# Kernel tuning notes

Hardware: AMD Instinct MI355X
Metric: run time of the kernel (lower is better)

The kernel has to match this reference:

```python
import jax, jax.numpy as jnp
import numpy as np

N = 50000      # nodes
E = 800000     # edges
F_IN = 128     # num_node_features
H = 128        # hidden_size
P = 128        # projection_dim
G = 512        # num graphs in batch


def setup_inputs() -> dict:
    key = jax.random.key(0)
    ks = jax.random.split(key, 16)
    def w(k, shape, fan_in):
        return (jax.random.normal(k, shape, jnp.float32) / np.float32(np.sqrt(fan_in)))
    inp = {
        "x": jax.random.normal(ks[0], (N, F_IN), jnp.float32),
        "edge_index": jax.random.randint(ks[1], (2, E), 0, N, dtype=jnp.int32),
        "batch": jnp.sort(jax.random.randint(ks[2], (N,), 0, G, dtype=jnp.int32)),
        "W_in": w(ks[3], (F_IN, H), F_IN), "b_in": jnp.zeros((H,), jnp.float32),
        "W1": w(ks[4], (H, H), H), "b1": jnp.zeros((H,), jnp.float32),
        "W2": w(ks[5], (H, H), H), "b2": jnp.zeros((H,), jnp.float32),
        "W3": w(ks[6], (H, H), H), "b3": jnp.zeros((H,), jnp.float32),
        "Wp1": w(ks[7], (3 * H, H), 3 * H), "bp1": jnp.zeros((H,), jnp.float32),
        "Wp2": w(ks[8], (H, P), H), "bp2": jnp.zeros((P,), jnp.float32),
    }
    return inp


def _gcn_conv(h_in, W, b, src, dst, dis):
    # GCNConv: D^-1/2 (A+I) D^-1/2 (X W) + b, edge weights = 1
    h = h_in @ W                                        # [N,H]
    norm = (dis[src] * dis[dst])[:, None]               # [E,1]
    msg = h[src] * norm                                 # gather + scale
    agg = jax.ops.segment_sum(msg, dst, num_segments=N)  # scatter-add
    agg = agg + h * (dis * dis)[:, None]                 # self-loop term
    return agg + b


def reference(x, edge_index, batch, W_in, b_in, W1, b1, W2, b2, W3, b3, Wp1, bp1, Wp2, bp2):
    src, dst = edge_index[0], edge_index[1]
    # degree with self-loops (target-side, symmetric norm)
    deg = jax.ops.segment_sum(jnp.ones((E,), jnp.float32), dst, num_segments=N) + 1.0
    dis = jax.lax.rsqrt(deg)                             # deg^-1/2, deg >= 1

    h = x @ W_in + b_in                                  # input projection
    r1 = jax.nn.relu(h + _gcn_conv(h, W1, b1, src, dst, dis))   # dropout = id (eval)
    r2 = jax.nn.relu(r1 + _gcn_conv(r1, W2, b2, src, dst, dis))
    r3 = jax.nn.relu(r2 + _gcn_conv(r2, W3, b3, src, dst, dis))

    jk = jnp.concatenate([r1, r2, r3], axis=1)           # JumpingKnowledge 'cat' -> [N,3H]
    sums = jax.ops.segment_sum(jk, batch, num_segments=G)
    cnts = jax.ops.segment_sum(jnp.ones((N,), jnp.float32), batch, num_segments=G)
    pooled = sums / jnp.maximum(cnts, 1.0)[:, None]      # global_mean_pool -> [G,3H]

    p = jax.nn.relu(pooled @ Wp1 + bp1) @ Wp2 + bp2      # projection head -> [G,P]
    nrm = jnp.sqrt(jnp.sum(p * p, axis=1, keepdims=True))
    return p / jnp.maximum(nrm, 1e-12)                   # F.normalize(dim=1)
```

## Files before the change

kernel.cpp:

```cpp
#include <hip/hip_runtime.h>
#include <hip/hip_bf16.h>


#define THREADS 256
#define BCAP 4096

typedef __attribute__((ext_vector_type(8))) short short8;
typedef __attribute__((ext_vector_type(4))) float f32x4;

static __device__ __forceinline__ unsigned short f2bf(float f) {
  unsigned u = __float_as_uint(f);
  u += 0x7fffu + ((u >> 16) & 1u);
  return (unsigned short)(u >> 16);
}
static __device__ __forceinline__ float bfval(unsigned short h) {
  return __uint_as_float((unsigned)h << 16);
}
static __device__ __forceinline__ float bf_lo(unsigned w) {
  return __uint_as_float(w << 16);
}
static __device__ __forceinline__ float bf_hi(unsigned w) {
  return __uint_as_float(w & 0xffff0000u);
}


__global__ __launch_bounds__(THREADS) void bucket_fill_kernel(
    const int* __restrict__ src, const int* __restrict__ dst,
    int* __restrict__ bkt_cursor, unsigned* __restrict__ edges_tmp, int E,
    const float* __restrict__ W0, const float* __restrict__ W1,
    const float* __restrict__ W2, const float* __restrict__ W3,
    unsigned short* __restrict__ Wtb) {
  __shared__ int hist[512];
  __shared__ int excl[512];
  __shared__ int gbase[512];
  __shared__ unsigned staging[2048];
  int t = threadIdx.x;
  int base = blockIdx.x * 2048;
  if (base >= E) {
    int cb = (E + 2047) >> 11;
    int tid = (blockIdx.x - cb) * THREADS + t;
    if (tid < 4 * 128 * 128) {
      int w = tid >> 14, c = (tid >> 7) & 127, k = tid & 127;
      const float* W = (w == 0) ? W0 : (w == 1) ? W1 : (w == 2) ? W2 : W3;
      float f = W[k * 128 + c];
      unsigned short hi = f2bf(f);
      unsigned short lo = f2bf(f - bfval(hi));
      int c16 = c >> 4, lc = c & 15;
      int ks = k >> 5, hq = (k >> 3) & 3, j = k & 7;
      int lane = hq * 16 + lc;
      size_t wb = (size_t)w * 32768;
      size_t fidx = (size_t)((c16 * 4 + ks) * 64 + lane) * 8 + j;
      Wtb[wb + fidx] = hi;
      Wtb[wb + 16384 + fidx] = lo;
    }
    return;
  }
  hist[t] = 0; hist[t + 256] = 0;
  __syncthreads();
  int e0 = base + t * 8;
  int ds[8], ss[8];
  if (e0 + 7 < E) {
    *(int4*)&ds[0] = *(const int4*)&dst[e0];
    *(int4*)&ds[4] = *(const int4*)&dst[e0 + 4];
    *(int4*)&ss[0] = *(const int4*)&src[e0];
    *(int4*)&ss[4] = *(const int4*)&src[e0 + 4];
  } else {
#pragma unroll
    for (int k = 0; k < 8; ++k) {
      ds[k] = (e0 + k < E) ? dst[e0 + k] : -1;
      ss[k] = (e0 + k < E) ? src[e0 + k] : 0;
    }
  }
  unsigned rec[8]; int bk[8]; int slot[8];
#pragma unroll
  for (int k = 0; k < 8; ++k) {
    bk[k] = -1;
    if (ds[k] >= 0) {
      rec[k] = ((unsigned)ds[k] << 16) | (unsigned)ss[k];
      bk[k] = ds[k] >> 7;
      slot[k] = atomicAdd(&hist[bk[k]], 1);
    }
  }
  __syncthreads();
  int v0 = hist[t], v1 = hist[t + 256];
  excl[t] = v0; excl[t + 256] = v1;
  __syncthreads();
  for (int off = 1; off < 512; off <<= 1) {
    int a = (t >= off) ? excl[t - off] : 0;
    int b = excl[t + 256 - off];
    __syncthreads();
    excl[t] += a; excl[t + 256] += b;
    __syncthreads();
  }
  int e0x = excl[t] - v0, e1x = excl[t + 256] - v1;
  __syncthreads();
  excl[t] = e0x; excl[t + 256] = e1x;
  __syncthreads();
#pragma unroll
  for (int k = 0; k < 8; ++k)
    if (bk[k] >= 0) staging[excl[bk[k]] + slot[k]] = rec[k];
  if (v0) gbase[t] = atomicAdd(&bkt_cursor[t], v0);
  if (v1) gbase[t + 256] = atomicAdd(&bkt_cursor[t + 256], v1);
  __syncthreads();
  int total = (base + 2048 <= E) ? 2048 : (E - base);
  for (int p = t; p < total; p += 256) {
    unsigned r = staging[p];
    int b = (int)(r >> 23);
    int pos = gbase[b] + (p - excl[b]);
    if (pos < BCAP)
      edges_tmp[(size_t)b * BCAP + pos] = r;
  }
}

__global__ __launch_bounds__(THREADS) void node_sort_kernel(
    const unsigned* __restrict__ edges_tmp, const int* __restrict__ bkt_cursor,
    const int* __restrict__ batch, int* __restrict__ row_beg,
    int* __restrict__ deg, float* __restrict__ dis,
    int* __restrict__ csr_src, int* __restrict__ g_off,
    unsigned* __restrict__ hwb_w, int N, int G) {
  __shared__ int lhist[128];
  __shared__ int lbase[128];
  __shared__ int lcur[128];
  int b = blockIdx.x, t = threadIdx.x;
  if (b == 0 && t >= 128 && t < 192)
    hwb_w[(size_t)N * 64 + (t - 128)] = 0;
  int cnt = bkt_cursor[b];
  if (cnt > BCAP) cnt = BCAP;
  size_t ebase = (size_t)b * BCAP;
  if (t < 128) lhist[t] = 0;
  __syncthreads();
  for (int p = t; p < cnt; p += 256)
    atomicAdd(&lhist[(edges_tmp[ebase + p] >> 16) & 127], 1);
  __syncthreads();
  int pad = 0;
  if (t < 128) {
    pad = (lhist[t] + 3) & ~3;
    lbase[t] = pad;
  }
  __syncthreads();
  for (int off = 1; off < 128; off <<= 1) {
    int a = (t >= off && t < 128) ? lbase[t - off] : 0;
    __syncthreads();
    if (t < 128) lbase[t] += a;
    __syncthreads();
  }
  if (t < 128) {
    int excl = lbase[t] - pad;
    int node = b * 128 + t;
    if (node < N) {
      row_beg[node] = (int)ebase + excl;
      deg[node] = lhist[t];
      dis[node] = rsqrtf((float)lhist[t] + 1.0f);
      for (int q = lhist[t]; q < pad; ++q)
        csr_src[ebase + excl + q] = N;
      int b0 = batch[node];
      int prev = (node == 0) ? -1 : batch[node - 1];
      for (int g = prev + 1; g <= b0; ++g) g_off[g] = node;
      if (node == N - 1)
        for (int g = b0 + 1; g <= G; ++g) g_off[g] = N;
    }
    lcur[t] = excl;
  }
  __syncthreads();
  for (int p = t; p < cnt; p += 256) {
    unsigned r = edges_tmp[ebase + p];
    int slot = atomicAdd(&lcur[(r >> 16) & 127], 1);
    csr_src[ebase + slot] = (int)(r & 0xffffu);
  }
}


__global__ __launch_bounds__(THREADS) void gemm_in_kernel(
    const float* __restrict__ A, const unsigned short* __restrict__ Wt0,
    const float* __restrict__ bias, const unsigned short* __restrict__ Wt1,
    const float* __restrict__ dis, float* __restrict__ hout,
    unsigned short* __restrict__ hwbout, int nrows) {
  __shared__ unsigned short lds[2][32][136];
  int t = threadIdx.x;
  int rbase = blockIdx.x * 32;
  if (rbase >= nrows) return;
#pragma unroll
  for (int i = 0; i < 4; ++i) {
    int fi = i * 256 + t;
    int row = fi >> 5;
    int c4 = fi & 31;
    int gr = rbase + row;
    f32x4 v = (gr < nrows) ? *(const f32x4*)&A[(size_t)gr * 128 + c4 * 4]
                           : (f32x4){0.f, 0.f, 0.f, 0.f};
    ushort4 hh, ll;
    unsigned short h0 = f2bf(v[0]); hh.x = h0; ll.x = f2bf(v[0] - bfval(h0));
    unsigned short h1 = f2bf(v[1]); hh.y = h1; ll.y = f2bf(v[1] - bfval(h1));
    unsigned short h2 = f2bf(v[2]); hh.z = h2; ll.z = f2bf(v[2] - bfval(h2));
    unsigned short h3 = f2bf(v[3]); hh.w = h3; ll.w = f2bf(v[3] - bfval(h3));
    *(ushort4*)&lds[0][row][c4 * 4] = hh;
    *(ushort4*)&lds[1][row][c4 * 4] = ll;
  }
  __syncthreads();
  int wave = t >> 6, lane = t & 63;
  int wr = wave >> 1, cw = wave & 1;
  int lrow = wr * 16 + (lane & 15);
  int hq = lane >> 4;
  int r = rbase + lrow;
  const short8* Wf0 = (const short8*)Wt0;
  const short8* Wf1 = (const short8*)Wt1;

  f32x4 acc[4];
#pragma unroll
  for (int i = 0; i < 4; ++i) acc[i] = (f32x4){0.f, 0.f, 0.f, 0.f};
#pragma unroll
  for (int ks = 0; ks < 4; ++ks) {
    short8 ahi = *(const short8*)&lds[0][lrow][ks * 32 + hq * 8];
    short8 alo = *(const short8*)&lds[1][lrow][ks * 32 + hq * 8];
#pragma unroll
    for (int i = 0; i < 4; ++i) {
      int c16 = cw * 4 + i;
      short8 wh = Wf0[(c16 * 4 + ks) * 64 + lane];
      short8 wl = Wf0[(32 + c16 * 4 + ks) * 64 + lane];
      acc[i] = __builtin_amdgcn_mfma_f32_16x16x32_bf16(wh, ahi, acc[i], 0, 0, 0);
      acc[i] = __builtin_amdgcn_mfma_f32_16x16x32_bf16(wl, ahi, acc[i], 0, 0, 0);
      acc[i] = __builtin_amdgcn_mfma_f32_16x16x32_bf16(wh, alo, acc[i], 0, 0, 0);
    }
  }
  __syncthreads();
#pragma unroll
  for (int i = 0; i < 4; ++i) {
    int fbase = cw * 64 + 16 * i + 4 * hq;
    f32x4 bb = *(const f32x4*)&bias[fbase];
    f32x4 hv;
#pragma unroll
    for (int j = 0; j < 4; ++j) hv[j] = acc[i][j] + bb[j];
    if (r < nrows)
      *(f32x4*)&hout[(size_t)r * 128 + fbase] = hv;
    ushort4 hh, ll;
    unsigned short q0 = f2bf(hv[0]); hh.x = q0; ll.x = f2bf(hv[0] - bfval(q0));
    unsigned short q1 = f2bf(hv[1]); hh.y = q1; ll.y = f2bf(hv[1] - bfval(q1));
    unsigned short q2 = f2bf(hv[2]); hh.z = q2; ll.z = f2bf(hv[2] - bfval(q2));
    unsigned short q3 = f2bf(hv[3]); hh.w = q3; ll.w = f2bf(hv[3] - bfval(q3));
    *(ushort4*)&lds[0][lrow][fbase] = hh;
    *(ushort4*)&lds[1][lrow][fbase] = ll;
  }
  __syncthreads();
#pragma unroll
  for (int i = 0; i < 4; ++i) acc[i] = (f32x4){0.f, 0.f, 0.f, 0.f};
#pragma unroll
  for (int ks = 0; ks < 4; ++ks) {
    short8 ahi = *(const short8*)&lds[0][lrow][ks * 32 + hq * 8];
    short8 alo = *(const short8*)&lds[1][lrow][ks * 32 + hq * 8];
#pragma unroll
    for (int i = 0; i < 4; ++i) {
      int c16 = cw * 4 + i;
      short8 wh = Wf1[(c16 * 4 + ks) * 64 + lane];
      short8 wl = Wf1[(32 + c16 * 4 + ks) * 64 + lane];
      acc[i] = __builtin_amdgcn_mfma_f32_16x16x32_bf16(wh, ahi, acc[i], 0, 0, 0);
      acc[i] = __builtin_amdgcn_mfma_f32_16x16x32_bf16(wl, ahi, acc[i], 0, 0, 0);
      acc[i] = __builtin_amdgcn_mfma_f32_16x16x32_bf16(wh, alo, acc[i], 0, 0, 0);
    }
  }
  if (r >= nrows) return;
  float sc = dis[r];
#pragma unroll
  for (int i = 0; i < 4; ++i) {
    int fbase = cw * 64 + 16 * i + 4 * hq;
    unsigned w0 = ((unsigned)f2bf(acc[i][1] * sc) << 16) |
                  (unsigned)f2bf(acc[i][0] * sc);
    unsigned w1 = ((unsigned)f2bf(acc[i][3] * sc) << 16) |
                  (unsigned)f2bf(acc[i][2] * sc);
    uint2 st; st.x = w0; st.y = w1;
    *(uint2*)&hwbout[(size_t)r * 128 + fbase] = st;
  }
}

template <int OUT_FP32>
__global__ __launch_bounds__(THREADS) void gemm_mfma(
    const float* __restrict__ A, const unsigned short* __restrict__ Wt,
    const float* __restrict__ bias, const float* __restrict__ scale,
    void* __restrict__ outv, int nrows) {
  __shared__ unsigned short lds[2][32][136];
  int t = threadIdx.x;
  int rbase = blockIdx.x * 32;
  if (rbase >= nrows) return;
#pragma unroll
  for (int i = 0; i < 4; ++i) {
    int fi = i * 256 + t;
    int row = fi >> 5;
    int c4 = fi & 31;
    int gr = rbase + row;
    f32x4 v = (gr < nrows) ? *(const f32x4*)&A[(size_t)gr * 128 + c4 * 4]
                           : (f32x4){0.f, 0.f, 0.f, 0.f};
    ushort4 hh, ll;
    unsigned short h0 = f2bf(v[0]); hh.x = h0; ll.x = f2bf(v[0] - bfval(h0));
    unsigned short h1 = f2bf(v[1]); hh.y = h1; ll.y = f2bf(v[1] - bfval(h1));
    unsigned short h2 = f2bf(v[2]); hh.z = h2; ll.z = f2bf(v[2] - bfval(h2));
    unsigned short h3 = f2bf(v[3]); hh.w = h3; ll.w = f2bf(v[3] - bfval(h3));
    *(ushort4*)&lds[0][row][c4 * 4] = hh;
    *(ushort4*)&lds[1][row][c4 * 4] = ll;
  }
  __syncthreads();
  int wave = t >> 6, lane = t & 63;
  int wr = wave >> 1, cw = wave & 1;
  int lrow = wr * 16 + (lane & 15);
  int hq = lane >> 4;
  int r = rbase + lrow;
  const short8* Wf = (const short8*)Wt;

  f32x4 acc[4];
#pragma unroll
  for (int i = 0; i < 4; ++i) acc[i] = (f32x4){0.f, 0.f, 0.f, 0.f};
#pragma unroll
  for (int ks = 0; ks < 4; ++ks) {
    short8 ahi = *(const short8*)&lds[0][lrow][ks * 32 + hq * 8];
    short8 alo = *(const short8*)&lds[1][lrow][ks * 32 + hq * 8];
#pragma unroll
    for (int i = 0; i < 4; ++i) {
      int c16 = cw * 4 + i;
      short8 wh = Wf[(c16 * 4 + ks) * 64 + lane];
      short8 wl = Wf[(32 + c16 * 4 + ks) * 64 + lane];
      acc[i] = __builtin_amdgcn_mfma_f32_16x16x32_bf16(wh, ahi, acc[i], 0, 0, 0);
      acc[i] = __builtin_amdgcn_mfma_f32_16x16x32_bf16(wl, ahi, acc[i], 0, 0, 0);
      acc[i] = __builtin_amdgcn_mfma_f32_16x16x32_bf16(wh, alo, acc[i], 0, 0, 0);
    }
  }
  if (r >= nrows) return;
  float sc = scale ? scale[r] : 1.0f;
#pragma unroll
  for (int i = 0; i < 4; ++i) {
    int fbase = cw * 64 + 16 * i + 4 * hq;
    float b4[4] = {0.f, 0.f, 0.f, 0.f};
    if (bias) {
      f32x4 bb = *(const f32x4*)&bias[fbase];
      b4[0] = bb[0]; b4[1] = bb[1]; b4[2] = bb[2]; b4[3] = bb[3];
    }
    if (OUT_FP32) {
      f32x4 o;
#pragma unroll
      for (int j = 0; j < 4; ++j) o[j] = (acc[i][j] + b4[j]) * sc;
      *(f32x4*)&((float*)outv)[(size_t)r * 128 + fbase] = o;
    } else {
      unsigned w0 = ((unsigned)f2bf((acc[i][1] + b4[1]) * sc) << 16) |
                    (unsigned)f2bf((acc[i][0] + b4[0]) * sc);
      unsigned w1 = ((unsigned)f2bf((acc[i][3] + b4[3]) * sc) << 16) |
                    (unsigned)f2bf((acc[i][2] + b4[2]) * sc);
      uint2 st; st.x = w0; st.y = w1;
      *(uint2*)&((unsigned short*)outv)[(size_t)r * 128 + fbase] = st;
    }
  }
}

__global__ __launch_bounds__(THREADS) void agg_kernel(
    const float* __restrict__ hin, const unsigned short* __restrict__ hwsb,
    const float* __restrict__ bias, const float* __restrict__ dis,
    const int* __restrict__ row_beg, const int* __restrict__ deg,
    const int* __restrict__ csr_src, float* __restrict__ out, int n) {
  int v = (blockIdx.x * THREADS + threadIdx.x) >> 6;
  int lane = threadIdx.x & 63;
  if (v >= n) return;
  int p = lane & 15;
  int qa = (lane >> 4) << 2;
  const char* hwB = (const char*)hwsb;
  float acc[8];
#pragma unroll
  for (int i = 0; i < 8; ++i) acc[i] = 0.f;
  int b = row_beg[v];
  int pc = (deg[v] + 3) & ~3;

  for (int chunk = 0; chunk < pc; chunk += 64) {
    int m = pc - chunk; if (m > 64) m = 64;
    int idx = csr_src[b + chunk + lane];
    for (int j = 0; j < m; j += 4) {
      int s = __builtin_amdgcn_ds_bpermute((j << 2) + qa, idx);
      uint4 w = *(const uint4*)(hwB + (size_t)s * 256 + p * 16);
      acc[0] += bf_lo(w.x); acc[1] += bf_hi(w.x);
      acc[2] += bf_lo(w.y); acc[3] += bf_hi(w.y);
      acc[4] += bf_lo(w.z); acc[5] += bf_hi(w.z);
      acc[6] += bf_lo(w.w); acc[7] += bf_hi(w.w);
    }
  }
#pragma unroll
  for (int i = 0; i < 8; ++i) {
    acc[i] += __shfl_xor(acc[i], 16, 64);
    acc[i] += __shfl_xor(acc[i], 32, 64);
  }
  if (lane < 16) {
    float dv = dis[v];
    uint4 sw = *(const uint4*)(hwB + (size_t)v * 256 + p * 16);
    float sf[8] = {bf_lo(sw.x), bf_hi(sw.x), bf_lo(sw.y), bf_hi(sw.y),
                   bf_lo(sw.z), bf_hi(sw.z), bf_lo(sw.w), bf_hi(sw.w)};
    f32x4 h0 = *(const f32x4*)&hin[(size_t)v * 128 + p * 8];
    f32x4 h1 = *(const f32x4*)&hin[(size_t)v * 128 + p * 8 + 4];
    f32x4 bb0 = *(const f32x4*)&bias[p * 8];
    f32x4 bb1 = *(const f32x4*)&bias[p * 8 + 4];
    f32x4 o0, o1;
#pragma unroll
    for (int j = 0; j < 4; ++j) {
      o0[j] = fmaxf(h0[j] + dv * (acc[j] + sf[j]) + bb0[j], 0.f);
      o1[j] = fmaxf(h1[j] + dv * (acc[4 + j] + sf[4 + j]) + bb1[j], 0.f);
    }
    *(f32x4*)&out[(size_t)v * 128 + p * 8] = o0;
    *(f32x4*)&out[(size_t)v * 128 + p * 8 + 4] = o1;
  }
}

__global__ __launch_bounds__(512) void pool_head_kernel(
    const float* __restrict__ r1, const float* __restrict__ r2,
    const float* __restrict__ r3, const int* __restrict__ g_off,
    const float* __restrict__ Wp1, const float* __restrict__ bp1,
    const float* __restrict__ Wp2, const float* __restrict__ bp2,
    float* __restrict__ out) {
  __shared__ float red[16][384];
  __shared__ float ps[384];
  __shared__ float t1[128];
  __shared__ float wsum[2];
  int g = blockIdx.x, t = threadIdx.x;
  int sub = t >> 5;
  int c4 = t & 31;
  int beg = g_off[g], end = g_off[g + 1];
  f32x4 s1 = {0.f, 0.f, 0.f, 0.f}, s2 = s1, s3 = s1;
  for (int i = beg + sub; i < end; i += 16) {
    size_t o = (size_t)i * 128 + c4 * 4;
    f32x4 a = *(const f32x4*)&r1[o];
    f32x4 b = *(const f32x4*)&r2[o];
    f32x4 c = *(const f32x4*)&r3[o];
#pragma unroll
    for (int j = 0; j < 4; ++j) { s1[j] += a[j]; s2[j] += b[j]; s3[j] += c[j]; }
  }
#pragma unroll
  for (int j = 0; j < 4; ++j) {
    red[sub][c4 * 4 + j] = s1[j];
    red[sub][128 + c4 * 4 + j] = s2[j];
    red[sub][256 + c4 * 4 + j] = s3[j];
  }
  __syncthreads();
  if (t < 384) {
    float inv = 1.0f / fmaxf((float)(end - beg), 1.0f);
    float s = 0.f;
#pragma unroll
    for (int k = 0; k < 16; ++k) s += red[k][t];
    ps[t] = s * inv;
  }
  __syncthreads();
  if (t < 128) {
    float acc = bp1[t];
    for (int k = 0; k < 384; ++k) acc += ps[k] * Wp1[k * 128 + t];
    t1[t] = fmaxf(acc, 0.f);
  }
  __syncthreads();
  if (t < 128) {
    float acc2 = bp2[t];
    for (int k = 0; k < 128; ++k) acc2 += t1[k] * Wp2[k * 128 + t];
    float ss = acc2 * acc2;
    for (int off = 32; off > 0; off >>= 1) ss += __shfl_down(ss, off, 64);
    if ((t & 63) == 0) wsum[t >> 6] = ss;
    __syncthreads();
    float nrm = sqrtf(wsum[0] + wsum[1]);
    out[g * 128 + t] = acc2 / fmaxf(nrm, 1e-12f);
  }
}

static inline size_t align256(size_t x) { return (x + 255) & ~(size_t)255; }

extern "C" void kernel_launch(void* const* d_in, const int* in_sizes, int n_in,
                              void* d_out, int out_size, void* d_ws, size_t ws_size,
                              hipStream_t stream) {
  const float* x     = (const float*)d_in[0];
  const int*   ei    = (const int*)d_in[1];
  const int*   batch = (const int*)d_in[2];
  const float* W_in  = (const float*)d_in[3];
  const float* b_in  = (const float*)d_in[4];
  const float* W1    = (const float*)d_in[5];
  const float* b1    = (const float*)d_in[6];
  const float* W2    = (const float*)d_in[7];
  const float* b2    = (const float*)d_in[8];
  const float* W3    = (const float*)d_in[9];
  const float* b3    = (const float*)d_in[10];
  const float* Wp1   = (const float*)d_in[11];
  const float* bp1   = (const float*)d_in[12];
  const float* Wp2   = (const float*)d_in[13];
  const float* bp2   = (const float*)d_in[14];
  float* out = (float*)d_out;

  const int N = in_sizes[0] / 128;
  const int E = in_sizes[1] / 2;
  const int G = out_size / 128;
  const int* src = ei;
  const int* dst = ei + E;
  const int NB = (N + 127) / 128;
  const int CBLKS = (E + 2047) / 2048;

  char* p = (char*)d_ws;
  auto carve = [&](size_t bytes) { char* r = p; p += align256(bytes); return (void*)r; };
  int*   bkt_cursor = (int*)carve((size_t)NB * 4);
  int*   g_off      = (int*)carve((size_t)(G + 1) * 4);
  int*   row_beg    = (int*)carve((size_t)N * 4);
  int*   deg        = (int*)carve((size_t)N * 4);
  unsigned* edges_tmp = (unsigned*)carve((size_t)NB * BCAP * 4);
  int*   csr_src    = (int*)carve((size_t)NB * BCAP * 4);
  float* dis        = (float*)carve((size_t)N * 4);
  unsigned short* Wtb = (unsigned short*)carve((size_t)4 * 2 * 128 * 128 * 2);
  float* h   = (float*)carve((size_t)N * 128 * 4);
  float* r1  = (float*)carve((size_t)N * 128 * 4);
  float* r2  = (float*)carve((size_t)N * 128 * 4);
  float* r3  = (float*)carve((size_t)N * 128 * 4);
  unsigned short* hwb = (unsigned short*)carve((size_t)(N + 1) * 128 * 2);
  (void)ws_size; (void)n_in;

  hipMemsetAsync(bkt_cursor, 0, (size_t)NB * 4, stream);

  bucket_fill_kernel<<<CBLKS + 256, THREADS, 0, stream>>>(
      src, dst, bkt_cursor, edges_tmp, E, W_in, W1, W2, W3, Wtb);
  node_sort_kernel<<<NB, THREADS, 0, stream>>>(
      edges_tmp, bkt_cursor, batch, row_beg, deg, dis, csr_src, g_off,
      (unsigned*)hwb, N, G);

  int gemmBlocks = (N + 31) / 32;
  int aggBlocks = (N + 3) / 4;

  const unsigned short* Wt0 = Wtb;
  const unsigned short* Wt1 = Wtb + 32768;
  const unsigned short* Wt2 = Wtb + 2 * 32768;
  const unsigned short* Wt3 = Wtb + 3 * 32768;

  gemm_in_kernel<<<gemmBlocks, THREADS, 0, stream>>>(
      x, Wt0, b_in, Wt1, dis, h, hwb, N);
  agg_kernel<<<aggBlocks, THREADS, 0, stream>>>(h, hwb, b1, dis, row_beg, deg, csr_src, r1, N);
  gemm_mfma<0><<<gemmBlocks, THREADS, 0, stream>>>(r1, Wt2, nullptr, dis, hwb, N);
  agg_kernel<<<aggBlocks, THREADS, 0, stream>>>(r1, hwb, b2, dis, row_beg, deg, csr_src, r2, N);
  gemm_mfma<0><<<gemmBlocks, THREADS, 0, stream>>>(r2, Wt3, nullptr, dis, hwb, N);
  agg_kernel<<<aggBlocks, THREADS, 0, stream>>>(r2, hwb, b3, dis, row_beg, deg, csr_src, r3, N);

  pool_head_kernel<<<G, 512, 0, stream>>>(r1, r2, r3, g_off, Wp1, bp1, Wp2, bp2, out);
}
```

Before: 232.9 us.

## Fuse GCN aggregation with next layer's MFMA GEMM using ping-pong buffers

Merges the neighbor aggregation of layers 1 and 2 with the following layer's bf16-split MFMA GEMM into one kernel. Each block aggregates 32 nodes (4 waves, 8 nodes each), writes the ReLU residual output to global memory, and stages it as hi/lo bf16 directly in LDS for the GEMM. This avoids re-reading r1/r2 from global memory and removes two kernel launches. Two hw buffers alternate because the GEMM output would otherwise overwrite rows other blocks are still gathering. The cost is lower parallelism in the aggregation phase (fewer, larger blocks with serial node loops) and load imbalance from varying node degrees.

```diff
diff --git a/kernel.cpp b/kernel.cpp
--- a/kernel.cpp
+++ b/kernel.cpp
@@ -117,13 +117,16 @@
     const int* __restrict__ batch, int* __restrict__ row_beg,
     int* __restrict__ deg, float* __restrict__ dis,
     int* __restrict__ csr_src, int* __restrict__ g_off,
-    unsigned* __restrict__ hwb_w, int N, int G) {
+    unsigned* __restrict__ hwbA_w, unsigned* __restrict__ hwbB_w,
+    int N, int G) {
   __shared__ int lhist[128];
   __shared__ int lbase[128];
   __shared__ int lcur[128];
   int b = blockIdx.x, t = threadIdx.x;
-  if (b == 0 && t >= 128 && t < 192)
-    hwb_w[(size_t)N * 64 + (t - 128)] = 0;
+  if (b == 0 && t >= 128 && t < 192) {
+    hwbA_w[(size_t)N * 64 + (t - 128)] = 0;
+    hwbB_w[(size_t)N * 64 + (t - 128)] = 0;
+  }
   int cnt = bkt_cursor[b];
   if (cnt > BCAP) cnt = BCAP;
   size_t ebase = (size_t)b * BCAP;
@@ -270,39 +273,93 @@
   }
 }
 
-template <int OUT_FP32>
-__global__ __launch_bounds__(THREADS) void gemm_mfma(
-    const float* __restrict__ A, const unsigned short* __restrict__ Wt,
-    const float* __restrict__ bias, const float* __restrict__ scale,
-    void* __restrict__ outv, int nrows) {
+__global__ __launch_bounds__(THREADS) void agg_gemm_kernel(
+    const float* __restrict__ hin, const unsigned short* __restrict__ hwsb,
+    const float* __restrict__ bias, const float* __restrict__ dis,
+    const int* __restrict__ row_beg, const int* __restrict__ deg,
+    const int* __restrict__ csr_src, float* __restrict__ rout,
+    const unsigned short* __restrict__ Wt, unsigned short* __restrict__ hwbout,
+    int n) {
   __shared__ unsigned short lds[2][32][136];
   int t = threadIdx.x;
+  int wave = t >> 6, lane = t & 63;
   int rbase = blockIdx.x * 32;
-  if (rbase >= nrows) return;
-#pragma unroll
-  for (int i = 0; i < 4; ++i) {
-    int fi = i * 256 + t;
-    int row = fi >> 5;
-    int c4 = fi & 31;
-    int gr = rbase + row;
-    f32x4 v = (gr < nrows) ? *(const f32x4*)&A[(size_t)gr * 128 + c4 * 4]
-                           : (f32x4){0.f, 0.f, 0.f, 0.f};
-    ushort4 hh, ll;
-    unsigned short h0 = f2bf(v[0]); hh.x = h0; ll.x = f2bf(v[0] - bfval(h0));
-    unsigned short h1 = f2bf(v[1]); hh.y = h1; ll.y = f2bf(v[1] - bfval(h1));
-    unsigned short h2 = f2bf(v[2]); hh.z = h2; ll.z = f2bf(v[2] - bfval(h2));
-    unsigned short h3 = f2bf(v[3]); hh.w = h3; ll.w = f2bf(v[3] - bfval(h3));
-    *(ushort4*)&lds[0][row][c4 * 4] = hh;
-    *(ushort4*)&lds[1][row][c4 * 4] = ll;
-  }
-  __syncthreads();
-  int wave = t >> 6, lane = t & 63;
+  int p = lane & 15;
+  int qa = (lane >> 4) << 2;
+  const char* hwB = (const char*)hwsb;
+
+  for (int i = 0; i < 8; ++i) {
+    int lnode = i * 4 + wave;
+    int v = rbase + lnode;
+    float acc[8];
+#pragma unroll
+    for (int k = 0; k < 8; ++k) acc[k] = 0.f;
+    if (v < n) {
+      int b = row_beg[v];
+      int pc = (deg[v] + 3) & ~3;
+      for (int chunk = 0; chunk < pc; chunk += 64) {
+        int m = pc - chunk; if (m > 64) m = 64;
+        int idx = csr_src[b + chunk + lane];
+        for (int j = 0; j < m; j += 4) {
+          int s = __builtin_amdgcn_ds_bpermute((j << 2) + qa, idx);
+          uint4 w = *(const uint4*)(hwB + (size_t)s * 256 + p * 16);
+          acc[0] += bf_lo(w.x); acc[1] += bf_hi(w.x);
+          acc[2] += bf_lo(w.y); acc[3] += bf_hi(w.y);
+          acc[4] += bf_lo(w.z); acc[5] += bf_hi(w.z);
+          acc[6] += bf_lo(w.w); acc[7] += bf_hi(w.w);
+        }
+      }
+#pragma unroll
+      for (int k = 0; k < 8; ++k) {
+        acc[k] += __shfl_xor(acc[k], 16, 64);
+        acc[k] += __shfl_xor(acc[k], 32, 64);
+      }
+      if (lane < 16) {
+        float dv = dis[v];
+        uint4 sw = *(const uint4*)(hwB + (size_t)v * 256 + p * 16);
+        float sf[8] = {bf_lo(sw.x), bf_hi(sw.x), bf_lo(sw.y), bf_hi(sw.y),
+                       bf_lo(sw.z), bf_hi(sw.z), bf_lo(sw.w), bf_hi(sw.w)};
+        f32x4 h0 = *(const f32x4*)&hin[(size_t)v * 128 + p * 8];
+        f32x4 h1 = *(const f32x4*)&hin[(size_t)v * 128 + p * 8 + 4];
+        f32x4 bb0 = *(const f32x4*)&bias[p * 8];
+        f32x4 bb1 = *(const f32x4*)&bias[p * 8 + 4];
+        f32x4 o0, o1;
+#pragma unroll
+        for (int j = 0; j < 4; ++j) {
+          o0[j] = fmaxf(h0[j] + dv * (acc[j] + sf[j]) + bb0[j], 0.f);
+          o1[j] = fmaxf(h1[j] + dv * (acc[4 + j] + sf[4 + j]) + bb1[j], 0.f);
+        }
+        *(f32x4*)&rout[(size_t)v * 128 + p * 8] = o0;
+        *(f32x4*)&rout[(size_t)v * 128 + p * 8 + 4] = o1;
+        ushort4 hh0, ll0, hh1, ll1;
+#pragma unroll
+        for (int j = 0; j < 4; ++j) {
+          unsigned short q0 = f2bf(o0[j]);
+          ((unsigned short*)&hh0)[j] = q0;
+          ((unsigned short*)&ll0)[j] = f2bf(o0[j] - bfval(q0));
+          unsigned short q1 = f2bf(o1[j]);
+          ((unsigned short*)&hh1)[j] = q1;
+          ((unsigned short*)&ll1)[j] = f2bf(o1[j] - bfval(q1));
+        }
+        *(ushort4*)&lds[0][lnode][p * 8] = hh0;
+        *(ushort4*)&lds[0][lnode][p * 8 + 4] = hh1;
+        *(ushort4*)&lds[1][lnode][p * 8] = ll0;
+        *(ushort4*)&lds[1][lnode][p * 8 + 4] = ll1;
+      }
+    } else if (lane < 16) {
+      ushort4 z = {0, 0, 0, 0};
+      *(ushort4*)&lds[0][lnode][p * 8] = z;
+      *(ushort4*)&lds[0][lnode][p * 8 + 4] = z;
+      *(ushort4*)&lds[1][lnode][p * 8] = z;
+      *(ushort4*)&lds[1][lnode][p * 8 + 4] = z;
+    }
+  }
+  __syncthreads();
   int wr = wave >> 1, cw = wave & 1;
   int lrow = wr * 16 + (lane & 15);
   int hq = lane >> 4;
   int r = rbase + lrow;
   const short8* Wf = (const short8*)Wt;
-
   f32x4 acc[4];
 #pragma unroll
   for (int i = 0; i < 4; ++i) acc[i] = (f32x4){0.f, 0.f, 0.f, 0.f};
@@ -320,29 +377,17 @@
       acc[i] = __builtin_amdgcn_mfma_f32_16x16x32_bf16(wh, alo, acc[i], 0, 0, 0);
     }
   }
-  if (r >= nrows) return;
-  float sc = scale ? scale[r] : 1.0f;
+  if (r >= n) return;
+  float sc = dis[r];
 #pragma unroll
   for (int i = 0; i < 4; ++i) {
     int fbase = cw * 64 + 16 * i + 4 * hq;
-    float b4[4] = {0.f, 0.f, 0.f, 0.f};
-    if (bias) {
-      f32x4 bb = *(const f32x4*)&bias[fbase];
-      b4[0] = bb[0]; b4[1] = bb[1]; b4[2] = bb[2]; b4[3] = bb[3];
-    }
-    if (OUT_FP32) {
-      f32x4 o;
-#pragma unroll
-      for (int j = 0; j < 4; ++j) o[j] = (acc[i][j] + b4[j]) * sc;
-      *(f32x4*)&((float*)outv)[(size_t)r * 128 + fbase] = o;
-    } else {
-      unsigned w0 = ((unsigned)f2bf((acc[i][1] + b4[1]) * sc) << 16) |
-                    (unsigned)f2bf((acc[i][0] + b4[0]) * sc);
-      unsigned w1 = ((unsigned)f2bf((acc[i][3] + b4[3]) * sc) << 16) |
-                    (unsigned)f2bf((acc[i][2] + b4[2]) * sc);
-      uint2 st; st.x = w0; st.y = w1;
-      *(uint2*)&((unsigned short*)outv)[(size_t)r * 128 + fbase] = st;
-    }
+    unsigned w0 = ((unsigned)f2bf(acc[i][1] * sc) << 16) |
+                  (unsigned)f2bf(acc[i][0] * sc);
+    unsigned w1 = ((unsigned)f2bf(acc[i][3] * sc) << 16) |
+                  (unsigned)f2bf(acc[i][2] * sc);
+    uint2 st; st.x = w0; st.y = w1;
+    *(uint2*)&hwbout[(size_t)r * 128 + fbase] = st;
   }
 }
 
@@ -362,7 +407,6 @@
   for (int i = 0; i < 8; ++i) acc[i] = 0.f;
   int b = row_beg[v];
   int pc = (deg[v] + 3) & ~3;
-
   for (int chunk = 0; chunk < pc; chunk += 64) {
     int m = pc - chunk; if (m > 64) m = 64;
     int idx = csr_src[b + chunk + lane];
@@ -500,7 +544,8 @@
   float* r1  = (float*)carve((size_t)N * 128 * 4);
   float* r2  = (float*)carve((size_t)N * 128 * 4);
   float* r3  = (float*)carve((size_t)N * 128 * 4);
-  unsigned short* hwb = (unsigned short*)carve((size_t)(N + 1) * 128 * 2);
+  unsigned short* hwbA = (unsigned short*)carve((size_t)(N + 1) * 128 * 2);
+  unsigned short* hwbB = (unsigned short*)carve((size_t)(N + 1) * 128 * 2);
   (void)ws_size; (void)n_in;
 
   hipMemsetAsync(bkt_cursor, 0, (size_t)NB * 4, stream);
@@ -509,9 +554,9 @@
       src, dst, bkt_cursor, edges_tmp, E, W_in, W1, W2, W3, Wtb);
   node_sort_kernel<<<NB, THREADS, 0, stream>>>(
       edges_tmp, bkt_cursor, batch, row_beg, deg, dis, csr_src, g_off,
-      (unsigned*)hwb, N, G);
-
-  int gemmBlocks = (N + 31) / 32;
+      (unsigned*)hwbA, (unsigned*)hwbB, N, G);
+
+  int tileBlocks = (N + 31) / 32;
   int aggBlocks = (N + 3) / 4;
 
   const unsigned short* Wt0 = Wtb;
@@ -519,13 +564,15 @@
   const unsigned short* Wt2 = Wtb + 2 * 32768;
   const unsigned short* Wt3 = Wtb + 3 * 32768;
 
-  gemm_in_kernel<<<gemmBlocks, THREADS, 0, stream>>>(
-      x, Wt0, b_in, Wt1, dis, h, hwb, N);
-  agg_kernel<<<aggBlocks, THREADS, 0, stream>>>(h, hwb, b1, dis, row_beg, deg, csr_src, r1, N);
-  gemm_mfma<0><<<gemmBlocks, THREADS, 0, stream>>>(r1, Wt2, nullptr, dis, hwb, N);
-  agg_kernel<<<aggBlocks, THREADS, 0, stream>>>(r1, hwb, b2, dis, row_beg, deg, csr_src, r2, N);
-  gemm_mfma<0><<<gemmBlocks, THREADS, 0, stream>>>(r2, Wt3, nullptr, dis, hwb, N);
-  agg_kernel<<<aggBlocks, THREADS, 0, stream>>>(r2, hwb, b3, dis, row_beg, deg, csr_src, r3, N);
-
-  pool_head_kernel<<<G, 512, 0, stream>>>(r1, r2, r3, g_off, Wp1, bp1, Wp2, bp2, out);
-}
+  gemm_in_kernel<<<tileBlocks, THREADS, 0, stream>>>(
+      x, Wt0, b_in, Wt1, dis, h, hwbA, N);
+  agg_gemm_kernel<<<tileBlocks, THREADS, 0, stream>>>(
+      h, hwbA, b1, dis, row_beg, deg, csr_src, r1, Wt2, hwbB, N);
+  agg_gemm_kernel<<<tileBlocks, THREADS, 0, stream>>>(
+      r1, hwbB, b2, dis, row_beg, deg, csr_src, r2, Wt3, hwbA, N);
+  agg_kernel<<<aggBlocks, THREADS, 0, stream>>>(
+      r2, hwbA, b3, dis, row_beg, deg, csr_src, r3, N);
+
+  pool_head_kernel<<<G, 512, 0, stream>>>(
+      r1, r2, r3, g_off, Wp1, bp1, Wp2, bp2, out);
+}
```

After: 258.1 us. +10.8%, slower.
